# Kernel tuning notes

Measured on AMD Instinct MI355X. Metric: run time of the kernel, lower is better.

## Reference

```python
import jax, jax.numpy as jnp
import numpy as np

D_MODEL = 1024
N_HEADS = 16
D_K = D_MODEL // N_HEADS  # 64
SCALE = 0.125             # attention_scale = 1/sqrt(d_k)
ROPE_BASE = 10000.0
NEG_INF = -1e30


def setup_inputs() -> dict:
    key = jax.random.key(0)
    k1, k2, k3 = jax.random.split(key, 3)
    B, S = 2, 2048
    x = jax.random.normal(k1, (B, S, D_MODEL), jnp.float32)
    # torch Linear(d_model, 3*d_model, bias=False): stored here as [in, out]
    w_qkv = jax.random.normal(k2, (D_MODEL, 3 * D_MODEL), jnp.float32) * (D_MODEL ** -0.5)
    w_o = jax.random.normal(k3, (D_MODEL, D_MODEL), jnp.float32) * (D_MODEL ** -0.5)
    return {"x": x, "w_qkv": w_qkv, "w_o": w_o}


def _rotary(x):
    # x: [B, H, S, D]; standard half-split rotary over sequence positions
    S, D = x.shape[2], x.shape[3]
    inv_freq = 1.0 / (ROPE_BASE ** (jnp.arange(0, D, 2, dtype=jnp.float32) / D))  # [D/2]
    freqs = jnp.arange(S, dtype=jnp.float32)[:, None] * inv_freq[None, :]          # [S, D/2]
    cos = jnp.cos(freqs)[None, None]  # [1,1,S,D/2]
    sin = jnp.sin(freqs)[None, None]
    x1, x2 = jnp.split(x, 2, axis=-1)
    return jnp.concatenate([x1 * cos + x2 * sin, -x1 * sin + x2 * cos], axis=-1).astype(x.dtype)


def reference(x, w_qkv, w_o):
    B, S, _ = x.shape
    qkv = x @ w_qkv                                        # [B,S,3*D_MODEL]
    qkv = qkv.reshape(B, S, 3, N_HEADS, D_K).transpose(2, 0, 3, 1, 4)  # [3,B,H,S,Dk]
    q, k, v = qkv[0], qkv[1], qkv[2]
    q = _rotary(q)
    k = _rotary(k)
    scores = jnp.einsum('bhqd,bhkd->bhqk', q, k) * SCALE   # [B,H,S,S]
    causal = jnp.tril(jnp.ones((S, S), dtype=bool))
    scores = jnp.where(causal, scores, NEG_INF)
    attn = jax.nn.softmax(scores, axis=-1)
    out = jnp.einsum('bhqk,bhkd->bhqd', attn, v)           # [B,H,S,Dk]
    out = out.transpose(0, 2, 1, 3).reshape(B, S, D_MODEL)
    return out @ w_o
```

## Files before the change

### kernel.cpp

```cpp
#include <hip/hip_runtime.h>

typedef short bf16x8 __attribute__((ext_vector_type(8)));
typedef short bf16x4 __attribute__((ext_vector_type(4)));
typedef float f32x4 __attribute__((ext_vector_type(4)));
typedef float f32x16 __attribute__((ext_vector_type(16)));
typedef int i32x4 __attribute__((ext_vector_type(4)));

#define DEVI static __device__ __forceinline__

DEVI unsigned short f2b(float f) {
  unsigned u = __float_as_uint(f);
  u += 0x7FFFu + ((u >> 16) & 1u);
  return (unsigned short)(u >> 16);
}

DEVI void gload16(const void* g, void* l) {
  __builtin_amdgcn_global_load_lds((const __attribute__((address_space(1))) void*)g,
                                   (__attribute__((address_space(3))) void*)l, 16, 0, 0);
}

DEVI void pl32swap(int a, int b, int& outa, int& outb) {
#if __has_builtin(__builtin_amdgcn_permlane32_swap)
  auto r = __builtin_amdgcn_permlane32_swap(a, b, false, false);
  outa = ((const int*)&r)[0];
  outb = ((const int*)&r)[1];
#else
  int bp = __shfl_xor(b, 32);
  int ap = __shfl_xor(a, 32);
  outa = (threadIdx.x & 32) ? bp : a;
  outb = (threadIdx.x & 32) ? b : ap;
#endif
}

DEVI float halfmax(float x) {
  int o0, o1;
  pl32swap(__float_as_int(x), __float_as_int(x), o0, o1);
  return fmaxf(__int_as_float(o0), __int_as_float(o1));
}
DEVI float halfsum(float x) {
  int o0, o1;
  pl32swap(__float_as_int(x), __float_as_int(x), o0, o1);
  return __int_as_float(o0) + __int_as_float(o1);
}

__global__ void rope_table_kernel(float2* __restrict__ cst) {
  int i = blockIdx.x * 256 + threadIdx.x;
  int s = i >> 5, j = i & 31;
  float inv = powf(10000.0f, -(float)j * (1.0f / 32.0f));
  float a = (float)s * inv;
  cst[i] = make_float2(cosf(a), sinf(a));
}

__global__ void cvt_x_kernel(const float* __restrict__ x, unsigned short* __restrict__ xb) {
  int i = blockIdx.x * 256 + threadIdx.x;
  float4 v = ((const float4*)x)[i];
  ushort4 o;
  o.x = f2b(v.x); o.y = f2b(v.y); o.z = f2b(v.z); o.w = f2b(v.w);
  ((ushort4*)xb)[i] = o;
}

__global__ void transpose_kernel(const float* __restrict__ W, unsigned short* __restrict__ WT,
                                 int K, int N) {
  __shared__ float tile[32][33];
  int n0 = blockIdx.x * 32, k0 = blockIdx.y * 32;
  int tx = threadIdx.x, ty = threadIdx.y;
#pragma unroll
  for (int i = 0; i < 32; i += 8)
    tile[ty + i][tx] = W[(size_t)(k0 + ty + i) * N + n0 + tx];
  __syncthreads();
#pragma unroll
  for (int i = 0; i < 32; i += 8)
    WT[(size_t)(n0 + ty + i) * K + k0 + tx] = f2b(tile[tx][ty + i]);
}

__global__ __launch_bounds__(512, 2) void gemm_qkv_kernel(
    const unsigned short* __restrict__ Xb, const unsigned short* __restrict__ WT,
    const float2* __restrict__ cst,
    unsigned short* __restrict__ Qb, unsigned short* __restrict__ Kb,
    unsigned short* __restrict__ VTb) {
  __shared__ unsigned short As[2][256 * 64];
  __shared__ unsigned short Bs[2][256 * 64];
  const int tid = threadIdx.x;
  const int lane = tid & 63, wid = tid >> 6;
  const int flat = blockIdx.y * 12 + blockIdx.x;
  const int nf = (flat & 7) * 24 + (flat >> 3);
  const int bx = nf % 12, by = nf / 12;
  const int m0 = by * 256, n0 = bx * 256;
  const int wr = wid >> 2, wc = wid & 3;
  const int srow = lane >> 3;
  const int scc = ((lane & 7) ^ srow) * 8;
  const int rx = lane & 7;

  f32x4 acc[8][4] = {};

  auto stageA = [&](int k0, int nb, int i) {
    const int c = i * 8 + wid;
    const int row = c * 8 + srow;
    gload16(Xb + (size_t)(m0 + row) * 1024 + k0 + scc, (char*)As[nb] + c * 1024);
  };
  auto stageB = [&](int k0, int nb, int i) {
    const int c = i * 8 + wid;
    const int row = c * 8 + srow;
    gload16(WT + (size_t)(n0 + row) * 1024 + k0 + scc, (char*)Bs[nb] + c * 1024);
  };
  auto loadA = [&](const unsigned short* Ab, int q, bf16x8 af[2][2]) {
#pragma unroll
    for (int kk = 0; kk < 2; ++kk) {
      const int cc = ((kk * 4 + (lane >> 4)) ^ rx) * 8;
#pragma unroll
      for (int miL = 0; miL < 2; ++miL)
        af[miL][kk] = *(const bf16x8*)&Ab[(wr * 128 + (q * 2 + miL) * 16 + (lane & 15)) * 64 + cc];
    }
  };

#define QKV_MFMA_QUAD(Q)                                                      \
  __builtin_amdgcn_s_barrier();                                               \
  asm volatile("s_waitcnt lgkmcnt(0)" ::: "memory");                          \
  __builtin_amdgcn_s_setprio(1);                                              \
  _Pragma("unroll") for (int kk = 0; kk < 2; ++kk)                            \
    _Pragma("unroll") for (int miL = 0; miL < 2; ++miL)                       \
      _Pragma("unroll") for (int ni = 0; ni < 4; ++ni)                        \
        acc[(Q) * 2 + miL][ni] = __builtin_amdgcn_mfma_f32_16x16x32_bf16(     \
            af[miL][kk], bf[ni][kk], acc[(Q) * 2 + miL][ni], 0, 0, 0);        \
  __builtin_amdgcn_s_setprio(0);                                              \
  __builtin_amdgcn_s_barrier();

#pragma unroll
  for (int i = 0; i < 4; ++i) stageB(0, 0, i);
#pragma unroll
  for (int i = 0; i < 4; ++i) stageA(0, 0, i);
#pragma unroll
  for (int i = 0; i < 4; ++i) stageB(64, 1, i);
  stageA(64, 1, 0); stageA(64, 1, 2);
  asm volatile("s_waitcnt vmcnt(6)" ::: "memory");
  __builtin_amdgcn_s_barrier();

  for (int t = 0; t < 16; ++t) {
    const int b = t & 1;
    const unsigned short* Ab = As[b];
    const unsigned short* Bb = Bs[b];
    const int k1 = (t + 1) * 64, k2 = (t + 2) * 64;
    bf16x8 bf[4][2], af[2][2];

#pragma unroll
    for (int kk = 0; kk < 2; ++kk) {
      const int cc = ((kk * 4 + (lane >> 4)) ^ rx) * 8;
#pragma unroll
      for (int ni = 0; ni < 4; ++ni)
        bf[ni][kk] = *(const bf16x8*)&Bb[(wc * 64 + ni * 16 + (lane & 15)) * 64 + cc];
    }
    loadA(Ab, 0, af);
    if (t + 1 < 16) { stageA(k1, b ^ 1, 1); stageA(k1, b ^ 1, 3); }
    QKV_MFMA_QUAD(0)

    loadA(Ab, 1, af);
    if (t + 2 < 16) { stageB(k2, b, 0); stageB(k2, b, 1); }
    QKV_MFMA_QUAD(1)

    loadA(Ab, 2, af);
    if (t + 2 < 16) { stageB(k2, b, 2); stageB(k2, b, 3); }
    QKV_MFMA_QUAD(2)

    loadA(Ab, 3, af);
    if (t + 2 < 16) { stageA(k2, b, 0); stageA(k2, b, 2); }
    __builtin_amdgcn_s_barrier();
    asm volatile("s_waitcnt lgkmcnt(0)" ::: "memory");
    __builtin_amdgcn_s_setprio(1);
#pragma unroll
    for (int kk = 0; kk < 2; ++kk)
#pragma unroll
      for (int miL = 0; miL < 2; ++miL)
#pragma unroll
        for (int ni = 0; ni < 4; ++ni)
          acc[6 + miL][ni] = __builtin_amdgcn_mfma_f32_16x16x32_bf16(
              af[miL][kk], bf[ni][kk], acc[6 + miL][ni], 0, 0, 0);
    __builtin_amdgcn_s_setprio(0);
    if (t + 2 < 16) asm volatile("s_waitcnt vmcnt(6)" ::: "memory");
    else            asm volatile("s_waitcnt vmcnt(0)" ::: "memory");
    __builtin_amdgcn_s_barrier();
  }
#undef QKV_MFMA_QUAD

  unsigned short* slab = (wid < 4) ? (&As[0][0] + wid * 8192)
                                   : (&Bs[0][0] + (wid - 4) * 8192);
  const int n_base = n0 + wc * 64;
  const int ty = n_base >> 10;
  const int h = (n_base & 1023) >> 6;
  const int qrow = (lane >> 4) << 2;
  const int l15 = lane & 15;
  const int rlane = lane >> 3, clane = lane & 7;

  if (ty < 2) {
    unsigned short* dst = (ty == 0) ? Qb : Kb;
#pragma unroll
    for (int g = 0; g < 2; ++g) {
      const int rowg = m0 + wr * 128 + g * 64;
      const int s_half = rowg & 2047, bb = rowg >> 11;
#pragma unroll
      for (int miL = 0; miL < 4; ++miL) {
        const int mi = g * 4 + miL;
        const int rl0 = miL * 16 + qrow;
#pragma unroll
        for (int r = 0; r < 4; ++r) {
#pragma unroll
          for (int ni = 0; ni < 2; ++ni) {
            const int j = ni * 16 + l15;
            const float2 cs = cst[(s_half + rl0 + r) * 32 + j];
            const float x1 = acc[mi][ni][r], x2 = acc[mi][ni + 2][r];
            slab[(rl0 + r) * 72 + j]      = f2b(x1 * cs.x + x2 * cs.y);
            slab[(rl0 + r) * 72 + j + 32] = f2b(-x1 * cs.y + x2 * cs.x);
          }
        }
      }
      unsigned short* dp = dst + ((size_t)(bb * 16 + h) * 2048 + s_half) * 64;
#pragma unroll
      for (int i = 0; i < 8; ++i) {
        const int row = i * 8 + rlane;
        const bf16x8 v = *(const bf16x8*)&slab[row * 72 + clane * 8];
        *(bf16x8*)&dp[row * 64 + clane * 8] = v;
      }
    }
  } else {
#pragma unroll
    for (int g = 0; g < 2; ++g) {
      const int rowg = m0 + wr * 128 + g * 64;
      const int s_half = rowg & 2047, bb = rowg >> 11;
#pragma unroll
      for (int miL = 0; miL < 4; ++miL) {
        const int mi = g * 4 + miL;
        const int rl0 = miL * 16 + qrow;
#pragma unroll
        for (int ni = 0; ni < 4; ++ni) {
          const int d = ni * 16 + l15;
#pragma unroll
          for (int r = 0; r < 4; ++r)
            slab[d * 72 + rl0 + r] = f2b(acc[mi][ni][r]);
        }
      }
      unsigned short* vp = VTb + (size_t)(bb * 16 + h) * 64 * 2048 + s_half;
#pragma unroll
      for (int i = 0; i < 8; ++i) {
        const int d = i * 8 + rlane;
        const bf16x8 v = *(const bf16x8*)&slab[d * 72 + clane * 8];
        *(bf16x8*)&vp[(size_t)d * 2048 + clane * 8] = v;
      }
    }
  }
}

DEVI void gemm_mainloop(const unsigned short* __restrict__ A, const unsigned short* __restrict__ B,
                        unsigned short* As, unsigned short* Bs,
                        int m0, int n0, int lane, int wid, int wr, int wc,
                        f32x4 acc[4][4]) {
  const int srow = lane >> 3;
  const int scc = ((lane & 7) ^ srow) * 8;
  const int rx = lane & 7;
  auto stage = [&](int k0, int nb) {
    unsigned short* Ad = As + nb * 8192;
    unsigned short* Bd = Bs + nb * 8192;
#pragma unroll
    for (int i = 0; i < 4; ++i) {
      const int c = i * 4 + wid;
      const int row = c * 8 + srow;
      gload16(A + (size_t)(m0 + row) * 1024 + k0 + scc, (char*)Ad + c * 1024);
      gload16(B + (size_t)(n0 + row) * 1024 + k0 + scc, (char*)Bd + c * 1024);
    }
  };
  auto compute = [&](int nb) {
    const unsigned short* Ab = As + nb * 8192;
    const unsigned short* Bb = Bs + nb * 8192;
#pragma unroll
    for (int kk = 0; kk < 64; kk += 32) {
      const int cc = (((kk >> 3) + (lane >> 4)) ^ rx) * 8;
      bf16x8 a[4], b[4];
#pragma unroll
      for (int mi = 0; mi < 4; ++mi)
        a[mi] = *(const bf16x8*)&Ab[(wr * 64 + mi * 16 + (lane & 15)) * 64 + cc];
#pragma unroll
      for (int ni = 0; ni < 4; ++ni)
        b[ni] = *(const bf16x8*)&Bb[(wc * 64 + ni * 16 + (lane & 15)) * 64 + cc];
      __builtin_amdgcn_s_setprio(1);
#pragma unroll
      for (int mi = 0; mi < 4; ++mi)
#pragma unroll
        for (int ni = 0; ni < 4; ++ni)
          acc[mi][ni] = __builtin_amdgcn_mfma_f32_16x16x32_bf16(a[mi], b[ni], acc[mi][ni], 0, 0, 0);
      __builtin_amdgcn_s_setprio(0);
    }
  };
  stage(0, 0);
  stage(64, 1);
  for (int t = 0; t < 15; ++t) {
    asm volatile("s_waitcnt vmcnt(8)" ::: "memory");
    __builtin_amdgcn_s_barrier();
    compute(t & 1);
    __builtin_amdgcn_s_barrier();
    if (t < 14) stage((t + 2) * 64, t & 1);
  }
  asm volatile("s_waitcnt vmcnt(0)" ::: "memory");
  __builtin_amdgcn_s_barrier();
  compute(1);
}

DEVI void stage128(const unsigned short* __restrict__ Kh, const unsigned short* __restrict__ Vh,
                   int kbase, unsigned char* buf, int tid) {
  const int r = tid >> 3, c = tid & 7, cc = c ^ (r & 7);
  const int dst = (tid & ~63) * 16;
#pragma unroll
  for (int q = 0; q < 2; ++q) {
    unsigned char* b = buf + q * 16384;
    gload16(Kh + (size_t)(kbase + q * 64 + r) * 64 + cc * 8, b + dst);
    gload16(Vh + (size_t)r * 2048 + kbase + q * 64 + cc * 8, b + 8192 + dst);
  }
}

DEVI void attn_sub(const unsigned char* __restrict__ bufK, const unsigned char* __restrict__ bufV,
                   const bf16x8 qf[4], int s32, int kglob, bool diag, int qg, int ln, int hi,
                   float& m2, float& l_run, f32x16& acc0, f32x16& acc1) {
  const float C = 0.125f * 1.44269504f;
  const int rx = ln & 7;
  bf16x8 kf[4];
#pragma unroll
  for (int j = 0; j < 4; ++j) {
    const int cc = (2 * j + hi) ^ rx;
    kf[j] = *(const bf16x8*)(bufK + (s32 * 32 + ln) * 128 + cc * 16);
  }
  bf16x8 v0[2], v1[2];
#pragma unroll
  for (int p = 0; p < 2; ++p) {
    const int cc = (4 * s32 + 2 * p + hi) ^ rx;
    v0[p] = *(const bf16x8*)(bufV + ln * 128 + cc * 16);
    v1[p] = *(const bf16x8*)(bufV + (ln + 32) * 128 + cc * 16);
  }

  f32x16 stv = {};
  __builtin_amdgcn_s_setprio(1);
  stv = __builtin_amdgcn_mfma_f32_32x32x16_bf16(kf[0], qf[0], stv, 0, 0, 0);
  stv = __builtin_amdgcn_mfma_f32_32x32x16_bf16(kf[1], qf[1], stv, 0, 0, 0);
  stv = __builtin_amdgcn_mfma_f32_32x32x16_bf16(kf[2], qf[2], stv, 0, 0, 0);
  stv = __builtin_amdgcn_mfma_f32_32x32x16_bf16(kf[3], qf[3], stv, 0, 0, 0);
  __builtin_amdgcn_s_setprio(0);

  float sraw[16];
#pragma unroll
  for (int r = 0; r < 16; ++r) sraw[r] = stv[r];
  if (diag) {
#pragma unroll
    for (int r = 0; r < 16; ++r) {
      const int kg = kglob + (r & 3) + ((r >> 2) << 3) + (hi << 2);
      if (kg > qg) sraw[r] = -1e30f;
    }
  }
  float mraw = sraw[0];
#pragma unroll
  for (int r = 1; r < 16; ++r) mraw = fmaxf(mraw, sraw[r]);
  const float mlc = mraw * C;
  if (__any(mlc > m2 + 11.5416f)) {
    const float mnew = fmaxf(m2, halfmax(mlc));
    const float sc = exp2f(m2 - mnew);
    l_run *= sc;
#pragma unroll
    for (int r = 0; r < 16; ++r) { acc0[r] *= sc; acc1[r] *= sc; }
    m2 = mnew;
  }
  float p[16], ps = 0.f;
#pragma unroll
  for (int r = 0; r < 16; ++r) { p[r] = exp2f(fmaf(sraw[r], C, -m2)); ps += p[r]; }
  l_run += ps;

  int cw[8];
#pragma unroll
  for (int i = 0; i < 8; ++i)
    asm("v_cvt_pk_bf16_f32 %0, %1, %2" : "=v"(cw[i]) : "v"(p[2 * i]), "v"(p[2 * i + 1]));
  int a0, a1, b0, b1, a2, a3, b2, b3;
  pl32swap(cw[0], cw[2], a0, b0);
  pl32swap(cw[1], cw[3], a1, b1);
  pl32swap(cw[4], cw[6], a2, b2);
  pl32swap(cw[5], cw[7], a3, b3);
  const bf16x8 pa0 = __builtin_bit_cast(bf16x8, (i32x4){a0, a1, b0, b1});
  const bf16x8 pa1 = __builtin_bit_cast(bf16x8, (i32x4){a2, a3, b2, b3});

  __builtin_amdgcn_s_setprio(1);
  acc0 = __builtin_amdgcn_mfma_f32_32x32x16_bf16(v0[0], pa0, acc0, 0, 0, 0);
  acc0 = __builtin_amdgcn_mfma_f32_32x32x16_bf16(v0[1], pa1, acc0, 0, 0, 0);
  acc1 = __builtin_amdgcn_mfma_f32_32x32x16_bf16(v1[0], pa0, acc1, 0, 0, 0);
  acc1 = __builtin_amdgcn_mfma_f32_32x32x16_bf16(v1[1], pa1, acc1, 0, 0, 0);
  __builtin_amdgcn_s_setprio(0);
}

DEVI void write_partial(float* M, int slot, const f32x16& a0, const f32x16& a1,
                        float m2, float l) {
#pragma unroll
  for (int r = 0; r < 16; ++r) { M[slot + r] = a0[r]; M[slot + 16 + r] = a1[r]; }
  M[slot + 32] = m2;
  M[slot + 33] = l;
}

DEVI void write_merged(unsigned short* __restrict__ Ob, const float* M, int slot,
                       const f32x16& acc0, const f32x16& acc1, float m2, float l_run,
                       int bh, int q0, int ln, int hi) {
  const float mp = M[slot + 32], lp = M[slot + 33];
  const float m = fmaxf(m2, mp);
  const float eo = exp2f(m2 - m), ep = exp2f(mp - m);
  const float il = 1.0f / (l_run * eo + lp * ep);
  const int b = bh >> 4, h = bh & 15;
  unsigned short* ob = Ob + ((size_t)(b * 2048 + q0 + ln)) * 1024 + h * 64;
#pragma unroll
  for (int g = 0; g < 4; ++g) {
    ushort4 o0, o1;
    o0.x = f2b((acc0[4 * g + 0] * eo + M[slot + 4 * g + 0] * ep) * il);
    o0.y = f2b((acc0[4 * g + 1] * eo + M[slot + 4 * g + 1] * ep) * il);
    o0.z = f2b((acc0[4 * g + 2] * eo + M[slot + 4 * g + 2] * ep) * il);
    o0.w = f2b((acc0[4 * g + 3] * eo + M[slot + 4 * g + 3] * ep) * il);
    o1.x = f2b((acc1[4 * g + 0] * eo + M[slot + 16 + 4 * g + 0] * ep) * il);
    o1.y = f2b((acc1[4 * g + 1] * eo + M[slot + 16 + 4 * g + 1] * ep) * il);
    o1.z = f2b((acc1[4 * g + 2] * eo + M[slot + 16 + 4 * g + 2] * ep) * il);
    o1.w = f2b((acc1[4 * g + 3] * eo + M[slot + 16 + 4 * g + 3] * ep) * il);
    *(ushort4*)&ob[8 * g + 4 * hi]      = o0;
    *(ushort4*)&ob[32 + 8 * g + 4 * hi] = o1;
  }
}

__global__ __launch_bounds__(512) void attn_kernel(
    const unsigned short* __restrict__ Qb, const unsigned short* __restrict__ Kb,
    const unsigned short* __restrict__ VTb, unsigned short* __restrict__ Ob) {
  __shared__ unsigned char smem[2][2][16384];
  const int tid = threadIdx.x;
  const int lane = tid & 63, wid = tid >> 6;
  const int ln = lane & 31, hi = lane >> 5;
  const int s = wid & 3, half = wid >> 2;
  const int bh = blockIdx.x;
  const int p = blockIdx.y;
  const int jA = 15 - p, jB = p;
  const unsigned short* Qh = Qb + (size_t)bh * 2048 * 64;
  const unsigned short* Kh = Kb + (size_t)bh * 2048 * 64;
  const unsigned short* Vh = VTb + (size_t)bh * 64 * 2048;

  f32x16 aA0 = {}, aA1 = {}, aB0 = {}, aB1 = {};
  float mA = -1e30f, lA = 0.f, mB = -1e30f, lB = 0.f;
  int it = 0;

  auto load_q = [&](int q0, bf16x8 qf[4]) {
    const unsigned short* pq = Qh + (size_t)(q0 + ln) * 64 + hi * 8;
#pragma unroll
    for (int t = 0; t < 4; ++t) qf[t] = *(const bf16x8*)(pq + t * 16);
  };
  auto run_phase = [&](int j, const bf16x8 qf[4], f32x16& acc0, f32x16& acc1,
                       float& m2, float& l_run, int q0, int nextFirst) {
    const int qg = q0 + ln;
    const int top = q0 >> 5;
    for (int kb = 0; kb <= j; ++kb, ++it) {
      const int nxt = (kb < j) ? (kb + 1) * 128 : nextFirst;
      if (nxt >= 0) stage128(Kh, Vh, nxt, &smem[(it + 1) & 1][0][0], tid);
      const unsigned char* bufK = &smem[it & 1][half][0];
      const unsigned char* bufV = bufK + 8192;
      const int t64 = 2 * kb + half;
#pragma unroll
      for (int s32 = 0; s32 < 2; ++s32) {
        const int g32 = 2 * t64 + s32;
        if (g32 <= top)
          attn_sub(bufK, bufV, qf, s32, g32 * 32, g32 == top, qg, ln, hi, m2, l_run, acc0, acc1);
      }
      __syncthreads();
    }
  };

  bf16x8 qfA[4];
  load_q(jA * 128 + s * 32, qfA);
  stage128(Kh, Vh, 0, &smem[0][0][0], tid);
  __syncthreads();
  run_phase(jA, qfA, aA0, aA1, mA, lA, jA * 128 + s * 32, 0);
  bf16x8 qfB[4];
  load_q(jB * 128 + s * 32, qfB);
  run_phase(jB, qfB, aB0, aB1, mB, lB, jB * 128 + s * 32, -1);

  lA = halfsum(lA);
  lB = halfsum(lB);

  float* M = (float*)&smem[0][0][0];
  const int slot = (s * 64 + lane) * 34;
  if (half == 1) write_partial(M, slot, aA0, aA1, mA, lA);
  __syncthreads();
  if (half == 0) write_merged(Ob, M, slot, aA0, aA1, mA, lA, bh, jA * 128 + s * 32, ln, hi);
  __syncthreads();
  if (half == 0) write_partial(M, slot, aB0, aB1, mB, lB);
  __syncthreads();
  if (half == 1) write_merged(Ob, M, slot, aB0, aB1, mB, lB, bh, jB * 128 + s * 32, ln, hi);
}

__global__ __launch_bounds__(256) void gemm_out_kernel(
    const unsigned short* __restrict__ Ob, const unsigned short* __restrict__ WoT,
    float* __restrict__ out) {
  __shared__ unsigned short As[2][128 * 64];
  __shared__ unsigned short Bs[2][128 * 64];
  const int lane = threadIdx.x & 63, wid = threadIdx.x >> 6;
  const int m0 = blockIdx.y * 128, n0 = blockIdx.x * 128;
  const int wr = wid >> 1, wc = wid & 1;
  f32x4 acc[4][4] = {};
  gemm_mainloop(Ob, WoT, &As[0][0], &Bs[0][0], m0, n0, lane, wid, wr, wc, acc);
#pragma unroll
  for (int mi = 0; mi < 4; ++mi) {
    const int mrow = m0 + wr * 64 + mi * 16 + ((lane >> 4) << 2);
#pragma unroll
    for (int ni = 0; ni < 4; ++ni) {
      const int n = n0 + wc * 64 + ni * 16 + (lane & 15);
#pragma unroll
      for (int r = 0; r < 4; ++r)
        out[(size_t)(mrow + r) * 1024 + n] = acc[mi][ni][r];
    }
  }
}

extern "C" void kernel_launch(void* const* d_in, const int* in_sizes, int n_in,
                              void* d_out, int out_size, void* d_ws, size_t ws_size,
                              hipStream_t stream) {
  const float* x     = (const float*)d_in[0];
  const float* w_qkv = (const float*)d_in[1];
  const float* w_o   = (const float*)d_in[2];
  float* out = (float*)d_out;
  char* ws = (char*)d_ws;

  const size_t MB = 1 << 20;
  float2* cst = (float2*)(ws);
  unsigned short* Xb  = (unsigned short*)(ws + (512 << 10));
  unsigned short* WqT = (unsigned short*)(ws + (512 << 10) + 8  * MB);
  unsigned short* WoT = (unsigned short*)(ws + (512 << 10) + 14 * MB);
  unsigned short* Qb  = (unsigned short*)(ws + (512 << 10) + 16 * MB);
  unsigned short* Kb  = (unsigned short*)(ws + (512 << 10) + 24 * MB);
  unsigned short* VTb = (unsigned short*)(ws + (512 << 10) + 32 * MB);
  unsigned short* Ob  = Xb;

  rope_table_kernel<<<dim3(256), dim3(256), 0, stream>>>(cst);
  cvt_x_kernel<<<dim3(4096), dim3(256), 0, stream>>>(x, Xb);
  transpose_kernel<<<dim3(96, 32), dim3(32, 8), 0, stream>>>(w_qkv, WqT, 1024, 3072);
  transpose_kernel<<<dim3(32, 32), dim3(32, 8), 0, stream>>>(w_o, WoT, 1024, 1024);
  gemm_qkv_kernel<<<dim3(12, 16), dim3(512), 0, stream>>>(Xb, WqT, cst, Qb, Kb, VTb);
  attn_kernel<<<dim3(32, 8), dim3(512), 0, stream>>>(Qb, Kb, VTb, Ob);
  gemm_out_kernel<<<dim3(8, 32), dim3(256), 0, stream>>>(Ob, WoT, out);
}
```

Baseline: 120.5 us.

## Split attention KV range across four wave groups per block with tree merge

The attention kernel moves from 512 to 1024 threads, so four wave groups each handle a different 64-key slice of a 256-key stage instead of two groups sharing 128 keys. Staging now loads 256 keys of K and V per iteration into 64KB double buffers, and the partial softmax states are combined through a shared-memory tree merge before output. This raises parallelism per query tile and halves the number of outer KV iterations, at the cost of more LDS, extra merge barriers, and heavier register pressure under launch_bounds(1024,4). Causal masking leaves more idle wave groups in the short phase.

```diff
diff --git a/kernel.cpp b/kernel.cpp
--- a/kernel.cpp
+++ b/kernel.cpp
@@ -302,15 +302,19 @@
   compute(1);
 }
 
-DEVI void stage128(const unsigned short* __restrict__ Kh, const unsigned short* __restrict__ Vh,
+DEVI void stage256(const unsigned short* __restrict__ Kh, const unsigned short* __restrict__ Vh,
                    int kbase, unsigned char* buf, int tid) {
-  const int r = tid >> 3, c = tid & 7, cc = c ^ (r & 7);
-  const int dst = (tid & ~63) * 16;
-#pragma unroll
-  for (int q = 0; q < 2; ++q) {
-    unsigned char* b = buf + q * 16384;
-    gload16(Kh + (size_t)(kbase + q * 64 + r) * 64 + cc * 8, b + dst);
-    gload16(Vh + (size_t)r * 2048 + kbase + q * 64 + cc * 8, b + 8192 + dst);
+#pragma unroll
+  for (int i = 0; i < 4; ++i) {
+    const int T = tid + i * 1024;
+    const int g = T >> 10;
+    const int rem = T & 1023;
+    const int rr = (rem & 511) >> 3, c = rem & 7, cc = c ^ (rr & 7);
+    unsigned char* dst = buf + (T & ~63) * 16;
+    if (rem < 512)
+      gload16(Kh + (size_t)(kbase + g * 64 + rr) * 64 + cc * 8, dst);
+    else
+      gload16(Vh + (size_t)rr * 2048 + kbase + g * 64 + cc * 8, dst);
   }
 }
 
@@ -396,96 +400,140 @@
   M[slot + 33] = l;
 }
 
-DEVI void write_merged(unsigned short* __restrict__ Ob, const float* M, int slot,
-                       const f32x16& acc0, const f32x16& acc1, float m2, float l_run,
-                       int bh, int q0, int ln, int hi) {
+DEVI void merge_state(const float* M, int slot, float& m, float& l,
+                      f32x16& a0, f32x16& a1) {
   const float mp = M[slot + 32], lp = M[slot + 33];
-  const float m = fmaxf(m2, mp);
-  const float eo = exp2f(m2 - m), ep = exp2f(mp - m);
-  const float il = 1.0f / (l_run * eo + lp * ep);
+  const float mn = fmaxf(m, mp);
+  const float eo = exp2f(m - mn), ep = exp2f(mp - mn);
+  l = l * eo + lp * ep;
+#pragma unroll
+  for (int r = 0; r < 16; ++r) {
+    a0[r] = a0[r] * eo + M[slot + r] * ep;
+    a1[r] = a1[r] * eo + M[slot + 16 + r] * ep;
+  }
+  m = mn;
+}
+
+DEVI void writeO(unsigned short* __restrict__ Ob, const f32x16& a0, const f32x16& a1,
+                 float l, int bh, int q0, int ln, int hi) {
+  const float il = 1.0f / l;
   const int b = bh >> 4, h = bh & 15;
   unsigned short* ob = Ob + ((size_t)(b * 2048 + q0 + ln)) * 1024 + h * 64;
 #pragma unroll
   for (int g = 0; g < 4; ++g) {
     ushort4 o0, o1;
-    o0.x = f2b((acc0[4 * g + 0] * eo + M[slot + 4 * g + 0] * ep) * il);
-    o0.y = f2b((acc0[4 * g + 1] * eo + M[slot + 4 * g + 1] * ep) * il);
-    o0.z = f2b((acc0[4 * g + 2] * eo + M[slot + 4 * g + 2] * ep) * il);
-    o0.w = f2b((acc0[4 * g + 3] * eo + M[slot + 4 * g + 3] * ep) * il);
-    o1.x = f2b((acc1[4 * g + 0] * eo + M[slot + 16 + 4 * g + 0] * ep) * il);
-    o1.y = f2b((acc1[4 * g + 1] * eo + M[slot + 16 + 4 * g + 1] * ep) * il);
-    o1.z = f2b((acc1[4 * g + 2] * eo + M[slot + 16 + 4 * g + 2] * ep) * il);
-    o1.w = f2b((acc1[4 * g + 3] * eo + M[slot + 16 + 4 * g + 3] * ep) * il);
+    o0.x = f2b(a0[4 * g + 0] * il); o0.y = f2b(a0[4 * g + 1] * il);
+    o0.z = f2b(a0[4 * g + 2] * il); o0.w = f2b(a0[4 * g + 3] * il);
+    o1.x = f2b(a1[4 * g + 0] * il); o1.y = f2b(a1[4 * g + 1] * il);
+    o1.z = f2b(a1[4 * g + 2] * il); o1.w = f2b(a1[4 * g + 3] * il);
     *(ushort4*)&ob[8 * g + 4 * hi]      = o0;
     *(ushort4*)&ob[32 + 8 * g + 4 * hi] = o1;
   }
 }
 
-__global__ __launch_bounds__(512) void attn_kernel(
+__global__ __launch_bounds__(1024, 4) void attn_kernel(
     const unsigned short* __restrict__ Qb, const unsigned short* __restrict__ Kb,
     const unsigned short* __restrict__ VTb, unsigned short* __restrict__ Ob) {
-  __shared__ unsigned char smem[2][2][16384];
+  __shared__ unsigned char smem[2][65536];
   const int tid = threadIdx.x;
   const int lane = tid & 63, wid = tid >> 6;
   const int ln = lane & 31, hi = lane >> 5;
-  const int s = wid & 3, half = wid >> 2;
+  const int s = wid & 3, qt = wid >> 2;
   const int bh = blockIdx.x;
   const int p = blockIdx.y;
   const int jA = 15 - p, jB = p;
   const unsigned short* Qh = Qb + (size_t)bh * 2048 * 64;
   const unsigned short* Kh = Kb + (size_t)bh * 2048 * 64;
   const unsigned short* Vh = VTb + (size_t)bh * 64 * 2048;
-
-  f32x16 aA0 = {}, aA1 = {}, aB0 = {}, aB1 = {};
-  float mA = -1e30f, lA = 0.f, mB = -1e30f, lB = 0.f;
-  int it = 0;
+  const int rA = (2 * jA + 5) >> 2;
+  const int rB = (2 * jB + 5) >> 2;
 
   auto load_q = [&](int q0, bf16x8 qf[4]) {
     const unsigned short* pq = Qh + (size_t)(q0 + ln) * 64 + hi * 8;
 #pragma unroll
     for (int t = 0; t < 4; ++t) qf[t] = *(const bf16x8*)(pq + t * 16);
   };
-  auto run_phase = [&](int j, const bf16x8 qf[4], f32x16& acc0, f32x16& acc1,
-                       float& m2, float& l_run, int q0, int nextFirst) {
-    const int qg = q0 + ln;
-    const int top = q0 >> 5;
-    for (int kb = 0; kb <= j; ++kb, ++it) {
-      const int nxt = (kb < j) ? (kb + 1) * 128 : nextFirst;
-      if (nxt >= 0) stage128(Kh, Vh, nxt, &smem[(it + 1) & 1][0][0], tid);
-      const unsigned char* bufK = &smem[it & 1][half][0];
+  const int slot = (s * 64 + lane) * 34;
+  int it = 0;
+
+  {
+    f32x16 a0 = {}, a1 = {};
+    float m2 = -1e30f, l = 0.f;
+    bf16x8 qf[4];
+    load_q(jA * 128 + s * 32, qf);
+    const int q0 = jA * 128 + s * 32, qg = q0 + ln, top = q0 >> 5;
+
+    stage256(Kh, Vh, 0, &smem[0][0], tid);
+    __syncthreads();
+    for (int kb = 0; kb < rA; ++kb, ++it) {
+      stage256(Kh, Vh, (kb + 1 < rA) ? (kb + 1) * 256 : 0, &smem[(it + 1) & 1][0], tid);
+      const unsigned char* bufK = &smem[it & 1][0] + qt * 16384;
       const unsigned char* bufV = bufK + 8192;
-      const int t64 = 2 * kb + half;
+      const int t64 = 4 * kb + qt;
 #pragma unroll
       for (int s32 = 0; s32 < 2; ++s32) {
         const int g32 = 2 * t64 + s32;
         if (g32 <= top)
-          attn_sub(bufK, bufV, qf, s32, g32 * 32, g32 == top, qg, ln, hi, m2, l_run, acc0, acc1);
+          attn_sub(bufK, bufV, qf, s32, g32 * 32, g32 == top, qg, ln, hi, m2, l, a0, a1);
       }
       __syncthreads();
     }
-  };
-
-  bf16x8 qfA[4];
-  load_q(jA * 128 + s * 32, qfA);
-  stage128(Kh, Vh, 0, &smem[0][0][0], tid);
-  __syncthreads();
-  run_phase(jA, qfA, aA0, aA1, mA, lA, jA * 128 + s * 32, 0);
-  bf16x8 qfB[4];
-  load_q(jB * 128 + s * 32, qfB);
-  run_phase(jB, qfB, aB0, aB1, mB, lB, jB * 128 + s * 32, -1);
-
-  lA = halfsum(lA);
-  lB = halfsum(lB);
-
-  float* M = (float*)&smem[0][0][0];
-  const int slot = (s * 64 + lane) * 34;
-  if (half == 1) write_partial(M, slot, aA0, aA1, mA, lA);
-  __syncthreads();
-  if (half == 0) write_merged(Ob, M, slot, aA0, aA1, mA, lA, bh, jA * 128 + s * 32, ln, hi);
-  __syncthreads();
-  if (half == 0) write_partial(M, slot, aB0, aB1, mB, lB);
-  __syncthreads();
-  if (half == 1) write_merged(Ob, M, slot, aB0, aB1, mB, lB, bh, jB * 128 + s * 32, ln, hi);
+    l = halfsum(l);
+
+    float* R = (float*)&smem[(rA + 1) & 1][0];
+    if (qt == 1) write_partial(R, slot, a0, a1, m2, l);
+    __syncthreads();
+    if (qt == 0) merge_state(R, slot, m2, l, a0, a1);
+    __syncthreads();
+    if (qt == 3) write_partial(R, slot, a0, a1, m2, l);
+    __syncthreads();
+    if (qt == 2) merge_state(R, slot, m2, l, a0, a1);
+    __syncthreads();
+    if (qt == 2) write_partial(R, slot, a0, a1, m2, l);
+    __syncthreads();
+    if (qt == 0) merge_state(R, slot, m2, l, a0, a1);
+    __syncthreads();
+    if (qt == 0) writeO(Ob, a0, a1, l, bh, q0, ln, hi);
+  }
+
+  {
+    f32x16 a0 = {}, a1 = {};
+    float m2 = -1e30f, l = 0.f;
+    bf16x8 qf[4];
+    load_q(jB * 128 + s * 32, qf);
+    const int q0 = jB * 128 + s * 32, qg = q0 + ln, top = q0 >> 5;
+
+    for (int kb = 0; kb < rB; ++kb, ++it) {
+      if (kb + 1 < rB) stage256(Kh, Vh, (kb + 1) * 256, &smem[(it + 1) & 1][0], tid);
+      const unsigned char* bufK = &smem[it & 1][0] + qt * 16384;
+      const unsigned char* bufV = bufK + 8192;
+      const int t64 = 4 * kb + qt;
+#pragma unroll
+      for (int s32 = 0; s32 < 2; ++s32) {
+        const int g32 = 2 * t64 + s32;
+        if (g32 <= top)
+          attn_sub(bufK, bufV, qf, s32, g32 * 32, g32 == top, qg, ln, hi, m2, l, a0, a1);
+      }
+      __syncthreads();
+    }
+    l = halfsum(l);
+
+    float* R = (float*)&smem[0][0];
+    if (qt == 1) write_partial(R, slot, a0, a1, m2, l);
+    __syncthreads();
+    if (qt == 0) merge_state(R, slot, m2, l, a0, a1);
+    __syncthreads();
+    if (qt == 3) write_partial(R, slot, a0, a1, m2, l);
+    __syncthreads();
+    if (qt == 2) merge_state(R, slot, m2, l, a0, a1);
+    __syncthreads();
+    if (qt == 2) write_partial(R, slot, a0, a1, m2, l);
+    __syncthreads();
+    if (qt == 0) {
+      merge_state(R, slot, m2, l, a0, a1);
+      writeO(Ob, a0, a1, l, bh, q0, ln, hi);
+    }
+  }
 }
 
 __global__ __launch_bounds__(256) void gemm_out_kernel(
@@ -535,6 +583,6 @@
   transpose_kernel<<<dim3(96, 32), dim3(32, 8), 0, stream>>>(w_qkv, WqT, 1024, 3072);
   transpose_kernel<<<dim3(32, 32), dim3(32, 8), 0, stream>>>(w_o, WoT, 1024, 1024);
   gemm_qkv_kernel<<<dim3(12, 16), dim3(512), 0, stream>>>(Xb, WqT, cst, Qb, Kb, VTb);
-  attn_kernel<<<dim3(32, 8), dim3(512), 0, stream>>>(Qb, Kb, VTb, Ob);
+  attn_kernel<<<dim3(32, 8), dim3(1024), 0, stream>>>(Qb, Kb, VTb, Ob);
   gemm_out_kernel<<<dim3(8, 32), dim3(256), 0, stream>>>(Ob, WoT, out);
 }
```

After: 120.7 us. Within noise of the previous version (+0.2%).
